# Kernel tuning notes

Measured on AMD Instinct MI355X. Metric: run time of the kernel, lower is better.

Reference implementation:

```python
import jax, jax.numpy as jnp
import numpy as np

LN_EPS = 1e-5

def _layer_norm(x, g, b):
    mu = jnp.mean(x, axis=-1, keepdims=True)
    var = jnp.mean(jnp.square(x - mu), axis=-1, keepdims=True)
    return (x - mu) * jax.lax.rsqrt(var + LN_EPS) * g + b

def _conv(x, src, tgt, N, alphas, ws, W3, W_self, bias, deg_power):
    # alphas, ws: tuples of 3 per-edge [E] arrays (sp, ctx, lat)
    # W3: [3, in, out]; deg_power: [3]
    out = x @ W_self + bias  # self loop + bias, [N, out]
    for c in range(3):
        eff = alphas[c] * ws[c]                                   # [E]
        deg = jnp.ones((N,), x.dtype).at[tgt].add(eff)            # [N]
        dinv = jnp.power(jnp.clip(deg, 1e-6), deg_power[c])       # [N]
        norm = eff * dinv[tgt] * dinv[src]                        # [E]
        h = x @ W3[c]                                             # [N, out] (linear => transform before gather)
        msg = norm[:, None] * h[src]                              # [E, out]
        out = out + jax.ops.segment_sum(msg, tgt, num_segments=N)
    return out

def setup_inputs() -> dict:
    N, E, D, L = 50000, 1000000, 128, 2
    key = jax.random.key(0)
    ks = jax.random.split(key, 16)
    scale = 1.0 / np.sqrt(D)
    inp = {
        "x": jax.random.normal(ks[0], (N, D), jnp.float32),
        "edge_index": jax.random.randint(ks[1], (2, E), 0, N, jnp.int32),
        "alpha_sp": jax.random.uniform(ks[2], (E,), jnp.float32),
        "alpha_ctx": jax.random.uniform(ks[3], (E,), jnp.float32),
        "alpha_lat": jax.random.uniform(ks[4], (E,), jnp.float32),
        "w_sp": jax.random.uniform(ks[5], (E,), jnp.float32),
        "w_ctx": jax.random.uniform(ks[6], (E,), jnp.float32),
        "w_lat": jax.random.uniform(ks[7], (E,), jnp.float32),
        # stacked per-layer params: [L, 3, in, out] for the three channel weights
        "W3": jax.random.normal(ks[8], (L, 3, D, D), jnp.float32) * scale,
        "W_self": jax.random.normal(ks[9], (L, D, D), jnp.float32) * scale,
        "bias": jnp.zeros((L, D), jnp.float32),
        "deg_power": jnp.full((L, 3), -0.5, jnp.float32),
        "ln_g": jnp.ones((D,), jnp.float32),
        "ln_b": jnp.zeros((D,), jnp.float32),
        "num_nodes": N,
    }
    return inp

def reference(x, edge_index, alpha_sp, alpha_ctx, alpha_lat, w_sp, w_ctx, w_lat,
              W3, W_self, bias, deg_power, ln_g, ln_b, num_nodes):
    N = num_nodes
    src, tgt = edge_index[0], edge_index[1]
    alphas = (alpha_sp, alpha_ctx, alpha_lat)
    ws = (w_sp, w_ctx, w_lat)
    L = W3.shape[0]
    h = x
    for i in range(L):
        h = _conv(h, src, tgt, N, alphas, ws, W3[i], W_self[i], bias[i], deg_power[i])
        if i < L - 1:
            h = _layer_norm(h, ln_g, ln_b)
            h = jax.nn.relu(h)
            # dropout: eval mode (identity)
    return h
```

## Files before the change

### kernel.cpp

```cpp
#include <hip/hip_runtime.h>
#include <hip/hip_bf16.h>

typedef short bf16x8 __attribute__((ext_vector_type(8)));
typedef float f32x4 __attribute__((ext_vector_type(4)));

static inline int cdiv(int a, int b){ return (a + b - 1) / b; }

__global__ void k_cnt(const int* __restrict__ tgt, int* __restrict__ cnt, int E){
    int e = blockIdx.x * 256 + threadIdx.x;
    if (e >= E) return;
    atomicAdd(&cnt[tgt[e]], 1);
}

__global__ void k_scan1(const int* __restrict__ cnt, int* __restrict__ rs,
                        int* __restrict__ bsum, int N){
    __shared__ int s[256];
    int i = blockIdx.x * 256 + threadIdx.x;
    int v = (i < N) ? cnt[i] : 0;
    s[threadIdx.x] = v;
    __syncthreads();
    for (int off = 1; off < 256; off <<= 1){
        int t = (threadIdx.x >= off) ? s[threadIdx.x - off] : 0;
        __syncthreads();
        s[threadIdx.x] += t;
        __syncthreads();
    }
    if (i < N) rs[i] = s[threadIdx.x] - v;
    if (threadIdx.x == 255) bsum[blockIdx.x] = s[255];
}

__global__ void k_scan2(int* __restrict__ bsum, int nb){
    __shared__ int s[256];
    int v = (threadIdx.x < nb) ? bsum[threadIdx.x] : 0;
    s[threadIdx.x] = v;
    __syncthreads();
    for (int off = 1; off < 256; off <<= 1){
        int t = (threadIdx.x >= off) ? s[threadIdx.x - off] : 0;
        __syncthreads();
        s[threadIdx.x] += t;
        __syncthreads();
    }
    if (threadIdx.x < nb) bsum[threadIdx.x] = s[threadIdx.x] - v;
}

__global__ void k_scan3(int* __restrict__ rs, int* __restrict__ nxt,
                        const int* __restrict__ bsum, int N, int E){
    int i = blockIdx.x * 256 + threadIdx.x;
    if (i < N){
        int v = rs[i] + bsum[blockIdx.x];
        rs[i] = v;
        nxt[i] = v;
    }
    if (i == 0) rs[N] = E;
}

__global__ void k_scatter(const int* __restrict__ src, const int* __restrict__ tgt,
                          const float* __restrict__ asp,
                          const float* __restrict__ actx,
                          const float* __restrict__ alat,
                          const float* __restrict__ wsp,
                          const float* __restrict__ wctx,
                          const float* __restrict__ wlat,
                          int* __restrict__ nxt,
                          float4* __restrict__ effo4, int E){
    int e = blockIdx.x * 256 + threadIdx.x;
    if (e >= E) return;
    int t = tgt[e];
    int pos = atomicAdd(&nxt[t], 1);
    float4 v;
    v.x = asp[e]  * wsp[e];
    v.y = actx[e] * wctx[e];
    v.z = alat[e] * wlat[e];
    v.w = __int_as_float(src[e]);
    effo4[pos] = v;
}

__global__ __launch_bounds__(256) void k_deg(
        const float4* __restrict__ effo4, const int* __restrict__ rs,
        const float* __restrict__ dp,
        float* __restrict__ dinv_all,
        int N, int L){
    int n = blockIdx.x * 256 + threadIdx.x;
    if (n >= N) return;
    int beg = rs[n], end = rs[n + 1];
    float s0 = 0.f, s1 = 0.f, s2 = 0.f;
    for (int i = beg; i < end; ++i){
        float4 v = effo4[i];
        s0 += v.x; s1 += v.y; s2 += v.z;
    }
    float d0 = fmaxf(1.f + s0, 1e-6f);
    float d1 = fmaxf(1.f + s1, 1e-6f);
    float d2 = fmaxf(1.f + s2, 1e-6f);
    for (int l = 0; l < L; ++l){
        size_t base = ((size_t)l * N + n) * 3;
        dinv_all[base + 0] = powf(d0, dp[l * 3 + 0]);
        dinv_all[base + 1] = powf(d1, dp[l * 3 + 1]);
        dinv_all[base + 2] = powf(d2, dp[l * 3 + 2]);
    }
}

__global__ void k_normv(const float4* __restrict__ effo4,
                        const float* __restrict__ dinv,
                        float4* __restrict__ nv, int E){
    int e = blockIdx.x * 256 + threadIdx.x;
    if (e >= E) return;
    float4 v = effo4[e];
    int s = __float_as_int(v.w);
    float4 o;
    o.x = v.x * dinv[3 * s + 0];
    o.y = v.y * dinv[3 * s + 1];
    o.z = v.z * dinv[3 * s + 2];
    o.w = v.w;
    nv[e] = o;
}

__global__ void k_x2bf(const float* __restrict__ x, __hip_bfloat16* __restrict__ Ap, int n){
    int i = blockIdx.x * 256 + threadIdx.x;
    if (i < n) Ap[(size_t)(i >> 7) * 512 + (i & 127)] = __float2bfloat16(x[i]);
}

__global__ void k_wcat(const float* __restrict__ Wself,
                       const float* __restrict__ W3,
                       __hip_bfloat16* __restrict__ BT){
    int i = blockIdx.x * 256 + threadIdx.x;
    int j = i >> 9, k = i & 511;
    float v;
    if (k < 128) v = Wself[k * 128 + j];
    else {
        int c = (k >> 7) - 1, kk = k & 127;
        v = W3[(c * 128 + kk) * 128 + j];
    }
    BT[i] = __float2bfloat16(v);
}

__global__ __launch_bounds__(256) void k_msg(
        __hip_bfloat16* __restrict__ Ap,
        const float4* __restrict__ nv,
        const int* __restrict__ rs,
        const float* __restrict__ dinv,
        int N){
    int w = threadIdx.x >> 6, lane = threadIdx.x & 63;
    int t = blockIdx.x * 4 + w;
    if (t >= N) return;
    float ax0 = 0.f, ay0 = 0.f, ax1 = 0.f, ay1 = 0.f, ax2 = 0.f, ay2 = 0.f;
    int beg = rs[t], end = rs[t + 1];
    int i = beg;
    for (; i + 4 <= end; i += 4){
        float4 n0 = nv[i], n1 = nv[i + 1], n2 = nv[i + 2], n3 = nv[i + 3];
        const __hip_bfloat162* p0 = (const __hip_bfloat162*)(Ap + (size_t)__float_as_int(n0.w) * 512);
        const __hip_bfloat162* p1 = (const __hip_bfloat162*)(Ap + (size_t)__float_as_int(n1.w) * 512);
        const __hip_bfloat162* p2 = (const __hip_bfloat162*)(Ap + (size_t)__float_as_int(n2.w) * 512);
        const __hip_bfloat162* p3 = (const __hip_bfloat162*)(Ap + (size_t)__float_as_int(n3.w) * 512);
        __hip_bfloat162 v0 = p0[lane], v1 = p1[lane], v2 = p2[lane], v3 = p3[lane];
        float2 f0 = __bfloat1622float2(v0);
        float2 f1 = __bfloat1622float2(v1);
        float2 f2 = __bfloat1622float2(v2);
        float2 f3 = __bfloat1622float2(v3);
        ax0 += n0.x * f0.x; ay0 += n0.x * f0.y;
        ax1 += n0.y * f0.x; ay1 += n0.y * f0.y;
        ax2 += n0.z * f0.x; ay2 += n0.z * f0.y;
        ax0 += n1.x * f1.x; ay0 += n1.x * f1.y;
        ax1 += n1.y * f1.x; ay1 += n1.y * f1.y;
        ax2 += n1.z * f1.x; ay2 += n1.z * f1.y;
        ax0 += n2.x * f2.x; ay0 += n2.x * f2.y;
        ax1 += n2.y * f2.x; ay1 += n2.y * f2.y;
        ax2 += n2.z * f2.x; ay2 += n2.z * f2.y;
        ax0 += n3.x * f3.x; ay0 += n3.x * f3.y;
        ax1 += n3.y * f3.x; ay1 += n3.y * f3.y;
        ax2 += n3.z * f3.x; ay2 += n3.z * f3.y;
    }
    for (; i < end; ++i){
        float4 n0 = nv[i];
        const __hip_bfloat162* p0 = (const __hip_bfloat162*)(Ap + (size_t)__float_as_int(n0.w) * 512);
        float2 f0 = __bfloat1622float2(p0[lane]);
        ax0 += n0.x * f0.x; ay0 += n0.x * f0.y;
        ax1 += n0.y * f0.x; ay1 += n0.y * f0.y;
        ax2 += n0.z * f0.x; ay2 += n0.z * f0.y;
    }
    float dt0 = dinv[3 * t], dt1 = dinv[3 * t + 1], dt2 = dinv[3 * t + 2];
    __hip_bfloat162* yo = (__hip_bfloat162*)(Ap + (size_t)t * 512 + 128) + lane;
    float2 r0 = {dt0 * ax0, dt0 * ay0};
    float2 r1 = {dt1 * ax1, dt1 * ay1};
    float2 r2 = {dt2 * ax2, dt2 * ay2};
    yo[0]   = __float22bfloat162_rn(r0);
    yo[64]  = __float22bfloat162_rn(r1);
    yo[128] = __float22bfloat162_rn(r2);
}

__global__ __launch_bounds__(256) void k_gemm(
        const __hip_bfloat16* __restrict__ A,
        const __hip_bfloat16* __restrict__ BT,
        const float* __restrict__ bias,
        float* __restrict__ outbuf,
        int M){
    __shared__ __hip_bfloat16 As[128 * 128];
    __shared__ __hip_bfloat16 Bs[128 * 128];
    const int tid = threadIdx.x;
    const int row0 = blockIdx.x * 128;
    const int w = tid >> 6, lane = tid & 63;
    const int wm = (w & 1) * 64, wn = (w >> 1) * 64;
    const int lm = lane & 15, lq = lane >> 4;

    f32x4 acc[4][4];
    #pragma unroll
    for (int mt = 0; mt < 4; ++mt)
        #pragma unroll
        for (int nt = 0; nt < 4; ++nt)
            acc[mt][nt] = {0.f, 0.f, 0.f, 0.f};

    for (int kt = 0; kt < 4; ++kt){
        #pragma unroll
        for (int it = 0; it < 8; ++it){
            int v = it * 256 + tid;
            int r = v >> 4, c = v & 15;
            int soff = r * 128 + ((c ^ (r & 15)) << 3);
            int4 av = {0, 0, 0, 0};
            if (row0 + r < M)
                av = *(const int4*)(A + (size_t)(row0 + r) * 512 + kt * 128 + (c << 3));
            *(int4*)(&As[soff]) = av;
            int4 bv = *(const int4*)(BT + (size_t)r * 512 + kt * 128 + (c << 3));
            *(int4*)(&Bs[soff]) = bv;
        }
        __syncthreads();

        #pragma unroll
        for (int kk = 0; kk < 4; ++kk){
            int kc = kk * 4 + lq;
            bf16x8 a[4], b[4];
            #pragma unroll
            for (int mt = 0; mt < 4; ++mt){
                int r = wm + mt * 16 + lm;
                a[mt] = *(const bf16x8*)(&As[r * 128 + ((kc ^ (r & 15)) << 3)]);
            }
            #pragma unroll
            for (int nt = 0; nt < 4; ++nt){
                int r = wn + nt * 16 + lm;
                b[nt] = *(const bf16x8*)(&Bs[r * 128 + ((kc ^ (r & 15)) << 3)]);
            }
            #pragma unroll
            for (int mt = 0; mt < 4; ++mt)
                #pragma unroll
                for (int nt = 0; nt < 4; ++nt)
                    acc[mt][nt] = __builtin_amdgcn_mfma_f32_16x16x32_bf16(
                        a[mt], b[nt], acc[mt][nt], 0, 0, 0);
        }
        __syncthreads();
    }

    #pragma unroll
    for (int mt = 0; mt < 4; ++mt){
        #pragma unroll
        for (int nt = 0; nt < 4; ++nt){
            int col = wn + nt * 16 + lm;
            #pragma unroll
            for (int r = 0; r < 4; ++r){
                int row = row0 + wm + mt * 16 + lq * 4 + r;
                if (row < M)
                    outbuf[(size_t)row * 128 + col] = acc[mt][nt][r] + bias[col];
            }
        }
    }
}

__global__ __launch_bounds__(256) void k_ln(
        const float* __restrict__ outbuf,
        const float* __restrict__ g,
        const float* __restrict__ b,
        __hip_bfloat16* __restrict__ Ap, int N){
    int w = threadIdx.x >> 6, lane = threadIdx.x & 63;
    int t = blockIdx.x * 4 + w;
    if (t >= N) return;
    const float* row = outbuf + (size_t)t * 128;
    float x0 = row[2 * lane], x1 = row[2 * lane + 1];
    float s = x0 + x1;
    #pragma unroll
    for (int off = 32; off; off >>= 1) s += __shfl_xor(s, off);
    float mu = s * (1.0f / 128.0f);
    float d0 = x0 - mu, d1 = x1 - mu;
    float ss = d0 * d0 + d1 * d1;
    #pragma unroll
    for (int off = 32; off; off >>= 1) ss += __shfl_xor(ss, off);
    float r = rsqrtf(ss * (1.0f / 128.0f) + 1e-5f);
    float y0 = fmaxf(d0 * r * g[2 * lane]     + b[2 * lane],     0.0f);
    float y1 = fmaxf(d1 * r * g[2 * lane + 1] + b[2 * lane + 1], 0.0f);
    float2 y = {y0, y1};
    *((__hip_bfloat162*)(Ap + (size_t)t * 512) + lane) = __float22bfloat162_rn(y);
}

extern "C" void kernel_launch(void* const* d_in, const int* in_sizes, int n_in,
                              void* d_out, int out_size, void* d_ws, size_t ws_size,
                              hipStream_t stream) {
    const float* x     = (const float*)d_in[0];
    const int*   ei    = (const int*)d_in[1];
    const float* asp   = (const float*)d_in[2];
    const float* actx  = (const float*)d_in[3];
    const float* alat  = (const float*)d_in[4];
    const float* wsp   = (const float*)d_in[5];
    const float* wctx  = (const float*)d_in[6];
    const float* wlat  = (const float*)d_in[7];
    const float* W3    = (const float*)d_in[8];
    const float* Wself = (const float*)d_in[9];
    const float* bias  = (const float*)d_in[10];
    const float* dpow  = (const float*)d_in[11];
    const float* lng   = (const float*)d_in[12];
    const float* lnb   = (const float*)d_in[13];

    const int N = in_sizes[0] / 128;
    const int E = in_sizes[1] / 2;
    const int L = in_sizes[8] / (3 * 128 * 128);
    const int* src = ei;
    const int* tgt = ei + E;

    char* p = (char*)d_ws;
    auto alloc = [&](size_t bytes) -> void* {
        void* r = (void*)p;
        p += (bytes + 255) & ~(size_t)255;
        return r;
    };
    int*    cnt      = (int*)   alloc((size_t)N * 4);
    int*    rs       = (int*)   alloc((size_t)(N + 1) * 4);
    int*    nxt      = (int*)   alloc((size_t)N * 4);
    int*    bsum     = (int*)   alloc(1024);
    float4* effo4    = (float4*)alloc((size_t)E * 16);
    float4* nv       = (float4*)alloc((size_t)E * 16);
    float*  dinv_all = (float*) alloc((size_t)L * N * 3 * 4);
    float*  outbuf   = (float*) alloc((size_t)N * 128 * 4);
    __hip_bfloat16* Ap = (__hip_bfloat16*)alloc((size_t)N * 512 * 2);
    __hip_bfloat16* BT = (__hip_bfloat16*)alloc((size_t)128 * 512 * 2);

    const int nb = cdiv(N, 256);

    hipMemsetAsync(cnt, 0, (size_t)N * 4, stream);
    k_cnt    <<<cdiv(E, 256), 256, 0, stream>>>(tgt, cnt, E);
    k_scan1  <<<nb, 256, 0, stream>>>(cnt, rs, bsum, N);
    k_scan2  <<<1,  256, 0, stream>>>(bsum, nb);
    k_scan3  <<<nb, 256, 0, stream>>>(rs, nxt, bsum, N, E);
    k_scatter<<<cdiv(E, 256), 256, 0, stream>>>(src, tgt, asp, actx, alat, wsp, wctx, wlat,
                                                nxt, effo4, E);
    k_deg    <<<cdiv(N, 256), 256, 0, stream>>>(effo4, rs, dpow, dinv_all, N, L);
    k_x2bf   <<<cdiv(N * 128, 256), 256, 0, stream>>>(x, Ap, N * 128);

    for (int l = 0; l < L; ++l){
        float* obuf = (l == L - 1) ? (float*)d_out : outbuf;
        const float* dinv_l = dinv_all + (size_t)l * N * 3;
        k_normv<<<cdiv(E, 256), 256, 0, stream>>>(effo4, dinv_l, nv, E);
        k_msg  <<<cdiv(N, 4), 256, 0, stream>>>(Ap, nv, rs, dinv_l, N);
        k_wcat <<<256, 256, 0, stream>>>(Wself + (size_t)l * 128 * 128,
                                         W3 + (size_t)l * 3 * 128 * 128, BT);
        k_gemm <<<cdiv(N, 128), 256, 0, stream>>>(Ap, BT, bias + l * 128, obuf, N);
        if (l < L - 1)
            k_ln<<<cdiv(N, 4), 256, 0, stream>>>(obuf, lng, lnb, Ap, N);
    }
}
```

Baseline: 429.3 us.

## Pack edge records into 8-byte bf16 format and batch per-layer prep kernels

Edge records shrink from a 16-byte float4 to an 8-byte uint2. The source index goes in 16 bits and the three edge weights are stored as bf16, which cuts the traffic in the scatter, degree, normalisation and message kernels. The per-layer normalisation and weight-concatenation kernels are hoisted out of the layer loop and run once for all layers, which needs L-sized buffers. The edge-count kernel is vectorised to four edges per thread, and the message loop is unrolled to eight edges with loads issued before the arithmetic. The 16-bit source index only works when N is below 65536, and bf16 edge weights lose precision compared with fp32.

```diff
diff --git a/kernel.cpp b/kernel.cpp
--- a/kernel.cpp
+++ b/kernel.cpp
@@ -6,10 +6,24 @@
 
 static inline int cdiv(int a, int b){ return (a + b - 1) / b; }
 
+__device__ __forceinline__ unsigned pack_bf16_hi(float v){
+    return ((unsigned)__bfloat16_as_ushort(__float2bfloat16(v))) << 16;
+}
+__device__ __forceinline__ float bf16hi_to_f32(unsigned bits_hi16){
+    return __uint_as_float(bits_hi16);
+}
+
 __global__ void k_cnt(const int* __restrict__ tgt, int* __restrict__ cnt, int E){
-    int e = blockIdx.x * 256 + threadIdx.x;
-    if (e >= E) return;
-    atomicAdd(&cnt[tgt[e]], 1);
+    int e0 = (blockIdx.x * 256 + threadIdx.x) * 4;
+    if (e0 + 3 < E){
+        int4 t = *(const int4*)(tgt + e0);
+        atomicAdd(&cnt[t.x], 1);
+        atomicAdd(&cnt[t.y], 1);
+        atomicAdd(&cnt[t.z], 1);
+        atomicAdd(&cnt[t.w], 1);
+    } else {
+        for (int e = e0; e < E; ++e) atomicAdd(&cnt[tgt[e]], 1);
+    }
 }
 
 __global__ void k_scan1(const int* __restrict__ cnt, int* __restrict__ rs,
@@ -62,21 +76,19 @@
                           const float* __restrict__ wctx,
                           const float* __restrict__ wlat,
                           int* __restrict__ nxt,
-                          float4* __restrict__ effo4, int E){
+                          uint2* __restrict__ effo, int E){
     int e = blockIdx.x * 256 + threadIdx.x;
     if (e >= E) return;
     int t = tgt[e];
     int pos = atomicAdd(&nxt[t], 1);
-    float4 v;
-    v.x = asp[e]  * wsp[e];
-    v.y = actx[e] * wctx[e];
-    v.z = alat[e] * wlat[e];
-    v.w = __int_as_float(src[e]);
-    effo4[pos] = v;
+    uint2 v;
+    v.x = (unsigned)src[e] | pack_bf16_hi(asp[e] * wsp[e]);
+    v.y = (pack_bf16_hi(actx[e] * wctx[e]) >> 16) | pack_bf16_hi(alat[e] * wlat[e]);
+    effo[pos] = v;
 }
 
 __global__ __launch_bounds__(256) void k_deg(
-        const float4* __restrict__ effo4, const int* __restrict__ rs,
+        const uint2* __restrict__ effo, const int* __restrict__ rs,
         const float* __restrict__ dp,
         float* __restrict__ dinv_all,
         int N, int L){
@@ -85,8 +97,10 @@
     int beg = rs[n], end = rs[n + 1];
     float s0 = 0.f, s1 = 0.f, s2 = 0.f;
     for (int i = beg; i < end; ++i){
-        float4 v = effo4[i];
-        s0 += v.x; s1 += v.y; s2 += v.z;
+        uint2 v = effo[i];
+        s0 += bf16hi_to_f32(v.x & 0xFFFF0000u);
+        s1 += bf16hi_to_f32(v.y << 16);
+        s2 += bf16hi_to_f32(v.y & 0xFFFF0000u);
     }
     float d0 = fmaxf(1.f + s0, 1e-6f);
     float d1 = fmaxf(1.f + s1, 1e-6f);
@@ -99,19 +113,26 @@
     }
 }
 
-__global__ void k_normv(const float4* __restrict__ effo4,
-                        const float* __restrict__ dinv,
-                        float4* __restrict__ nv, int E){
-    int e = blockIdx.x * 256 + threadIdx.x;
-    if (e >= E) return;
-    float4 v = effo4[e];
-    int s = __float_as_int(v.w);
-    float4 o;
-    o.x = v.x * dinv[3 * s + 0];
-    o.y = v.y * dinv[3 * s + 1];
-    o.z = v.z * dinv[3 * s + 2];
-    o.w = v.w;
-    nv[e] = o;
+__global__ void k_normv(const uint2* __restrict__ effo,
+                        const float* __restrict__ dinv_all,
+                        uint2* __restrict__ nv, int E, int N, int L){
+    int i = blockIdx.x * 256 + threadIdx.x;
+    if (i >= L * E) return;
+    int l = i / E;
+    int e = i - l * E;
+    const float* dinv = dinv_all + (size_t)l * N * 3;
+    uint2 v = effo[e];
+    unsigned s = v.x & 0xFFFFu;
+    float e0 = bf16hi_to_f32(v.x & 0xFFFF0000u);
+    float e1 = bf16hi_to_f32(v.y << 16);
+    float e2 = bf16hi_to_f32(v.y & 0xFFFF0000u);
+    float n0 = e0 * dinv[3 * s + 0];
+    float n1 = e1 * dinv[3 * s + 1];
+    float n2 = e2 * dinv[3 * s + 2];
+    uint2 o;
+    o.x = s | pack_bf16_hi(n0);
+    o.y = (pack_bf16_hi(n1) >> 16) | pack_bf16_hi(n2);
+    nv[i] = o;
 }
 
 __global__ void k_x2bf(const float* __restrict__ x, __hip_bfloat16* __restrict__ Ap, int n){
@@ -121,21 +142,24 @@
 
 __global__ void k_wcat(const float* __restrict__ Wself,
                        const float* __restrict__ W3,
-                       __hip_bfloat16* __restrict__ BT){
-    int i = blockIdx.x * 256 + threadIdx.x;
-    int j = i >> 9, k = i & 511;
+                       __hip_bfloat16* __restrict__ BT,
+                       int L){
+    int i = blockIdx.x * 256 + threadIdx.x;
+    if (i >= L * 65536) return;
+    int l = i >> 16, r = i & 65535;
+    int j = r >> 9, k = r & 511;
     float v;
-    if (k < 128) v = Wself[k * 128 + j];
+    if (k < 128) v = Wself[l * 16384 + k * 128 + j];
     else {
         int c = (k >> 7) - 1, kk = k & 127;
-        v = W3[(c * 128 + kk) * 128 + j];
+        v = W3[l * 49152 + (c * 128 + kk) * 128 + j];
     }
     BT[i] = __float2bfloat16(v);
 }
 
 __global__ __launch_bounds__(256) void k_msg(
         __hip_bfloat16* __restrict__ Ap,
-        const float4* __restrict__ nv,
+        const uint2* __restrict__ nv,
         const int* __restrict__ rs,
         const float* __restrict__ dinv,
         int N){
@@ -145,37 +169,38 @@
     float ax0 = 0.f, ay0 = 0.f, ax1 = 0.f, ay1 = 0.f, ax2 = 0.f, ay2 = 0.f;
     int beg = rs[t], end = rs[t + 1];
     int i = beg;
-    for (; i + 4 <= end; i += 4){
-        float4 n0 = nv[i], n1 = nv[i + 1], n2 = nv[i + 2], n3 = nv[i + 3];
-        const __hip_bfloat162* p0 = (const __hip_bfloat162*)(Ap + (size_t)__float_as_int(n0.w) * 512);
-        const __hip_bfloat162* p1 = (const __hip_bfloat162*)(Ap + (size_t)__float_as_int(n1.w) * 512);
-        const __hip_bfloat162* p2 = (const __hip_bfloat162*)(Ap + (size_t)__float_as_int(n2.w) * 512);
-        const __hip_bfloat162* p3 = (const __hip_bfloat162*)(Ap + (size_t)__float_as_int(n3.w) * 512);
-        __hip_bfloat162 v0 = p0[lane], v1 = p1[lane], v2 = p2[lane], v3 = p3[lane];
-        float2 f0 = __bfloat1622float2(v0);
-        float2 f1 = __bfloat1622float2(v1);
-        float2 f2 = __bfloat1622float2(v2);
-        float2 f3 = __bfloat1622float2(v3);
-        ax0 += n0.x * f0.x; ay0 += n0.x * f0.y;
-        ax1 += n0.y * f0.x; ay1 += n0.y * f0.y;
-        ax2 += n0.z * f0.x; ay2 += n0.z * f0.y;
-        ax0 += n1.x * f1.x; ay0 += n1.x * f1.y;
-        ax1 += n1.y * f1.x; ay1 += n1.y * f1.y;
-        ax2 += n1.z * f1.x; ay2 += n1.z * f1.y;
-        ax0 += n2.x * f2.x; ay0 += n2.x * f2.y;
-        ax1 += n2.y * f2.x; ay1 += n2.y * f2.y;
-        ax2 += n2.z * f2.x; ay2 += n2.z * f2.y;
-        ax0 += n3.x * f3.x; ay0 += n3.x * f3.y;
-        ax1 += n3.y * f3.x; ay1 += n3.y * f3.y;
-        ax2 += n3.z * f3.x; ay2 += n3.z * f3.y;
+    for (; i + 8 <= end; i += 8){
+        uint2 m[8];
+        #pragma unroll
+        for (int u = 0; u < 8; ++u) m[u] = nv[i + u];
+        float2 f[8];
+        #pragma unroll
+        for (int u = 0; u < 8; ++u){
+            const __hip_bfloat162* p =
+                (const __hip_bfloat162*)(Ap + (size_t)(m[u].x & 0xFFFFu) * 512);
+            f[u] = __bfloat1622float2(p[lane]);
+        }
+        #pragma unroll
+        for (int u = 0; u < 8; ++u){
+            float n0 = bf16hi_to_f32(m[u].x & 0xFFFF0000u);
+            float n1 = bf16hi_to_f32(m[u].y << 16);
+            float n2 = bf16hi_to_f32(m[u].y & 0xFFFF0000u);
+            ax0 += n0 * f[u].x; ay0 += n0 * f[u].y;
+            ax1 += n1 * f[u].x; ay1 += n1 * f[u].y;
+            ax2 += n2 * f[u].x; ay2 += n2 * f[u].y;
+        }
     }
     for (; i < end; ++i){
-        float4 n0 = nv[i];
-        const __hip_bfloat162* p0 = (const __hip_bfloat162*)(Ap + (size_t)__float_as_int(n0.w) * 512);
-        float2 f0 = __bfloat1622float2(p0[lane]);
-        ax0 += n0.x * f0.x; ay0 += n0.x * f0.y;
-        ax1 += n0.y * f0.x; ay1 += n0.y * f0.y;
-        ax2 += n0.z * f0.x; ay2 += n0.z * f0.y;
+        uint2 m = nv[i];
+        const __hip_bfloat162* p =
+            (const __hip_bfloat162*)(Ap + (size_t)(m.x & 0xFFFFu) * 512);
+        float2 fv = __bfloat1622float2(p[lane]);
+        float n0 = bf16hi_to_f32(m.x & 0xFFFF0000u);
+        float n1 = bf16hi_to_f32(m.y << 16);
+        float n2 = bf16hi_to_f32(m.y & 0xFFFF0000u);
+        ax0 += n0 * fv.x; ay0 += n0 * fv.y;
+        ax1 += n1 * fv.x; ay1 += n1 * fv.y;
+        ax2 += n2 * fv.x; ay2 += n2 * fv.y;
     }
     float dt0 = dinv[3 * t], dt1 = dinv[3 * t + 1], dt2 = dinv[3 * t + 2];
     __hip_bfloat162* yo = (__hip_bfloat162*)(Ap + (size_t)t * 512 + 128) + lane;
@@ -317,37 +342,37 @@
         p += (bytes + 255) & ~(size_t)255;
         return r;
     };
-    int*    cnt      = (int*)   alloc((size_t)N * 4);
-    int*    rs       = (int*)   alloc((size_t)(N + 1) * 4);
-    int*    nxt      = (int*)   alloc((size_t)N * 4);
-    int*    bsum     = (int*)   alloc(1024);
-    float4* effo4    = (float4*)alloc((size_t)E * 16);
-    float4* nv       = (float4*)alloc((size_t)E * 16);
-    float*  dinv_all = (float*) alloc((size_t)L * N * 3 * 4);
-    float*  outbuf   = (float*) alloc((size_t)N * 128 * 4);
+    int*   cnt      = (int*)  alloc((size_t)N * 4);
+    int*   rs       = (int*)  alloc((size_t)(N + 1) * 4);
+    int*   nxt      = (int*)  alloc((size_t)N * 4);
+    int*   bsum     = (int*)  alloc(1024);
+    uint2* effo     = (uint2*)alloc((size_t)E * 8);
+    uint2* nv       = (uint2*)alloc((size_t)L * E * 8);
+    float* dinv_all = (float*)alloc((size_t)L * N * 3 * 4);
+    float* outbuf   = (float*)alloc((size_t)N * 128 * 4);
     __hip_bfloat16* Ap = (__hip_bfloat16*)alloc((size_t)N * 512 * 2);
-    __hip_bfloat16* BT = (__hip_bfloat16*)alloc((size_t)128 * 512 * 2);
+    __hip_bfloat16* BT = (__hip_bfloat16*)alloc((size_t)L * 128 * 512 * 2);
 
     const int nb = cdiv(N, 256);
 
     hipMemsetAsync(cnt, 0, (size_t)N * 4, stream);
-    k_cnt    <<<cdiv(E, 256), 256, 0, stream>>>(tgt, cnt, E);
+    k_cnt    <<<cdiv(E, 1024), 256, 0, stream>>>(tgt, cnt, E);
     k_scan1  <<<nb, 256, 0, stream>>>(cnt, rs, bsum, N);
     k_scan2  <<<1,  256, 0, stream>>>(bsum, nb);
     k_scan3  <<<nb, 256, 0, stream>>>(rs, nxt, bsum, N, E);
     k_scatter<<<cdiv(E, 256), 256, 0, stream>>>(src, tgt, asp, actx, alat, wsp, wctx, wlat,
-                                                nxt, effo4, E);
-    k_deg    <<<cdiv(N, 256), 256, 0, stream>>>(effo4, rs, dpow, dinv_all, N, L);
+                                                nxt, effo, E);
+    k_deg    <<<cdiv(N, 256), 256, 0, stream>>>(effo, rs, dpow, dinv_all, N, L);
     k_x2bf   <<<cdiv(N * 128, 256), 256, 0, stream>>>(x, Ap, N * 128);
+    k_wcat   <<<cdiv(L * 65536, 256), 256, 0, stream>>>(Wself, W3, BT, L);
+    k_normv  <<<cdiv(L * E, 256), 256, 0, stream>>>(effo, dinv_all, nv, E, N, L);
 
     for (int l = 0; l < L; ++l){
         float* obuf = (l == L - 1) ? (float*)d_out : outbuf;
         const float* dinv_l = dinv_all + (size_t)l * N * 3;
-        k_normv<<<cdiv(E, 256), 256, 0, stream>>>(effo4, dinv_l, nv, E);
-        k_msg  <<<cdiv(N, 4), 256, 0, stream>>>(Ap, nv, rs, dinv_l, N);
-        k_wcat <<<256, 256, 0, stream>>>(Wself + (size_t)l * 128 * 128,
-                                         W3 + (size_t)l * 3 * 128 * 128, BT);
-        k_gemm <<<cdiv(N, 128), 256, 0, stream>>>(Ap, BT, bias + l * 128, obuf, N);
+        k_msg  <<<cdiv(N, 4), 256, 0, stream>>>(Ap, nv + (size_t)l * E, rs, dinv_l, N);
+        k_gemm <<<cdiv(N, 128), 256, 0, stream>>>(Ap, BT + (size_t)l * 65536,
+                                                  bias + l * 128, obuf, N);
         if (l < L - 1)
             k_ln<<<cdiv(N, 4), 256, 0, stream>>>(obuf, lng, lnb, Ap, N);
     }
```

After: 416.8 us. 1.03x faster.
